# Optimization experiments

Hardware: AMD Instinct MI355X
Metric: run time of the kernel (lower is better)

Reference implementation:

```python
import jax, jax.numpy as jnp
import numpy as np

N_NODES = 100000
N_EDGES = 1600000
F_IN = 256
DIM = 128
N_CLASSES = 16


def gcn_conv(x, W, b, src, dst, num_nodes):
    # PyG GCNConv: add self-loops, symmetric normalization D^-1/2 (A+I) D^-1/2,
    # linear transform then scatter-add aggregation at destination nodes.
    loops = jnp.arange(num_nodes)
    s = jnp.concatenate([src, loops])
    d = jnp.concatenate([dst, loops])
    deg = jax.ops.segment_sum(jnp.ones(d.shape[0], dtype=x.dtype), d, num_segments=num_nodes)
    dinv = jnp.where(deg > 0, jax.lax.rsqrt(deg), jnp.zeros_like(deg))
    norm = dinv[s] * dinv[d]                       # [E+N]
    h = x @ W                                      # [N, out] transform-then-propagate
    msg = h[s] * norm[:, None]                     # gather + scale
    out = jax.ops.segment_sum(msg, d, num_segments=num_nodes)  # scatter-add
    return out + b


def setup_inputs() -> dict:
    key = jax.random.key(0)
    k1, k2, k3, k4 = jax.random.split(key, 4)
    x = jax.random.normal(k1, (N_NODES, F_IN), dtype=jnp.float32)
    edge_index = jax.random.randint(k2, (2, N_EDGES), 0, N_NODES, dtype=jnp.int64)
    W1 = jax.random.normal(k3, (F_IN, DIM), dtype=jnp.float32) * 0.05
    b1 = jnp.zeros((DIM,), dtype=jnp.float32)
    W2 = jax.random.normal(k4, (DIM, N_CLASSES), dtype=jnp.float32) * 0.05
    b2 = jnp.zeros((N_CLASSES,), dtype=jnp.float32)
    return {"x": x, "edge_index": edge_index, "W1": W1, "b1": b1, "W2": W2, "b2": b2}


def reference(x, edge_index, W1, b1, W2, b2):
    # Gcn.forward with num_layers=2 (gcs empty), eval-mode dropout (identity)
    src, dst = edge_index[0], edge_index[1]
    n = x.shape[0]
    h = jax.nn.relu(gcn_conv(x, W1, b1, src, dst, n))
    logits = gcn_conv(h, W2, b2, src, dst, n)
    return jax.nn.log_softmax(logits, axis=-1)
```

## Files before the change

kernel.cpp:

```cpp
#include <hip/hip_runtime.h>
#include <hip/hip_bf16.h>

#define F_IN   256
#define DIM    128
#define NCLS   16
#define BSH    9
#define NBMAX  256
#define CAP    10240
#define PCAP   18432

typedef short bf16x8 __attribute__((ext_vector_type(8)));
typedef float f32x4  __attribute__((ext_vector_type(4)));
typedef float f32x2  __attribute__((ext_vector_type(2)));

__device__ __forceinline__ unsigned short f2bf(float f) {
    union { float f; unsigned u; } v; v.f = f;
    unsigned r = v.u + 0x7fffu + ((v.u >> 16) & 1u);
    return (unsigned short)(r >> 16);
}
__device__ __forceinline__ float bflo(unsigned v) { return __uint_as_float(v << 16); }
__device__ __forceinline__ float bfhi(unsigned v) { return __uint_as_float(v & 0xffff0000u); }

__global__ void init_kernel(const float* __restrict__ W1, unsigned short* __restrict__ W1f,
                            int* __restrict__ bucketCur,
                            unsigned* __restrict__ h1dummy, unsigned* __restrict__ h2dummy,
                            float* __restrict__ dinv, int N) {
    int t = blockIdx.x * blockDim.x + threadIdx.x;
    if (blockIdx.x == 0) {
        bucketCur[threadIdx.x] = threadIdx.x * CAP;
        if (threadIdx.x < 32) h1dummy[threadIdx.x] = 0;
        else if (threadIdx.x < 40) h2dummy[threadIdx.x - 32] = 0;
        else if (threadIdx.x == 40) dinv[N] = 0.f;
    }
    if (t >= 8 * 32 * 16 * 8) return;
    int j = t & 7, c = (t >> 3) & 15, g = (t >> 7) & 31, f = t >> 12;
    W1f[t] = f2bf(W1[(g * 8 + j) * DIM + f * 16 + c]);
}

__global__ __launch_bounds__(1024) void part_kernel(const int* __restrict__ src,
                                                    const int* __restrict__ dst,
                                                    int* __restrict__ bucketCur,
                                                    int2* __restrict__ pairs, int E) {
    __shared__ int hist[NBMAX];
    __shared__ int pos[NBMAX];
    int t = threadIdx.x;
    int base = blockIdx.x * 8192;
    int s[8], d[8];
#pragma unroll
    for (int k = 0; k < 8; k++) {
        int i = base + k * 1024 + t;
        bool v = (i < E);
        s[k] = v ? src[i] : 0;
        d[k] = v ? dst[i] : -1;
    }
    if (t < NBMAX) hist[t] = 0;
    __syncthreads();
#pragma unroll
    for (int k = 0; k < 8; k++)
        if (d[k] >= 0) atomicAdd(&hist[d[k] >> BSH], 1);
    __syncthreads();
    if (t < NBMAX && hist[t]) pos[t] = atomicAdd(&bucketCur[t], hist[t]);
    __syncthreads();
#pragma unroll
    for (int k = 0; k < 8; k++)
        if (d[k] >= 0) {
            int p = atomicAdd(&pos[d[k] >> BSH], 1);
            pairs[p] = make_int2(s[k], d[k]);
        }
}

__global__ __launch_bounds__(512) void csr_gemm_kernel(
        const int2* __restrict__ pairs, const int* __restrict__ bucketCur,
        int* __restrict__ rowInfo, float* __restrict__ dinv, int* __restrict__ col,
        const float* __restrict__ X, const unsigned short* __restrict__ W1f,
        unsigned char* __restrict__ H1, int N, int nbCsr) {
    __shared__ int sh[16384];
    int t = threadIdx.x;

    if (blockIdx.x < nbCsr) {
        int* cnt  = sh;
        int* part = sh + 512;
        int b = blockIdx.x;
        int n0 = b << BSH;
        int nn = N - n0; if (nn > 512) nn = 512;
        int in0 = b * CAP;
        int inEnd = bucketCur[b];
        int out0 = b * PCAP;

        cnt[t] = 0;
        __syncthreads();
        for (int p = in0 + t; p < inEnd; p += 512)
            atomicAdd(&cnt[pairs[p].y - n0], 1);
        __syncthreads();

        int c0 = cnt[t];
        int p0 = (c0 + 15) & ~15;
        part[t] = p0;
        __syncthreads();
        for (int off = 1; off < 512; off <<= 1) {
            int u = (t >= off) ? part[t - off] : 0;
            __syncthreads();
            part[t] += u;
            __syncthreads();
        }
        int e0 = out0 + part[t] - p0;
        __syncthreads();
        if (t < nn) {
            rowInfo[n0 + t] = ((e0 >> 4) << 12) | (p0 >> 4);
            dinv[n0 + t] = rsqrtf((float)(c0 + 1));
        }
        cnt[t] = e0;
        __syncthreads();

        for (int p = in0 + t; p < inEnd; p += 512) {
            int2 e = pairs[p];
            int q = atomicAdd(&cnt[e.y - n0], 1);
            col[q] = e.x;
        }
        __syncthreads();
        if (t < nn) for (int q = c0; q < p0; q++) col[e0 + q] = N;
    } else {
        int gb = blockIdx.x - nbCsr;
        int wm = t >> 6, l = t & 63;
        int lr = l & 15, lg = l >> 4;
        int bm = gb * 128 + wm * 16;

        int r = bm + lr;
        r = (r < N) ? r : (N - 1);
        const float* xp = X + (size_t)r * F_IN + lg * 8;

        float4 u[16];
#pragma unroll
        for (int s = 0; s < 8; s++) {
            u[2 * s + 0] = *(const float4*)(xp + s * 32);
            u[2 * s + 1] = *(const float4*)(xp + s * 32 + 4);
        }

        uint4* wv = (uint4*)sh;
        const uint4* wg = (const uint4*)W1f;
#pragma unroll
        for (int i = 0; i < 8; i++) wv[t + i * 512] = wg[t + i * 512];
        __syncthreads();
        const unsigned short* w1s = (const unsigned short*)sh;

        f32x4 acc[8];
#pragma unroll
        for (int f = 0; f < 8; f++) acc[f] = (f32x4){0.f, 0.f, 0.f, 0.f};

#pragma unroll
        for (int s = 0; s < 8; s++) {
            float4 u0 = u[2 * s + 0];
            float4 u1 = u[2 * s + 1];
            bf16x8 a;
            a[0] = (short)f2bf(u0.x); a[1] = (short)f2bf(u0.y);
            a[2] = (short)f2bf(u0.z); a[3] = (short)f2bf(u0.w);
            a[4] = (short)f2bf(u1.x); a[5] = (short)f2bf(u1.y);
            a[6] = (short)f2bf(u1.z); a[7] = (short)f2bf(u1.w);
#pragma unroll
            for (int f = 0; f < 8; f++) {
                bf16x8 b = *(const bf16x8*)(w1s + ((((f * 32 + s * 4 + lg) * 16) + lr) << 3));
                acc[f] = __builtin_amdgcn_mfma_f32_16x16x32_bf16(a, b, acc[f], 0, 0, 0);
            }
        }
#pragma unroll
        for (int rr = 0; rr < 4; rr++) {
            int row = bm + lg * 4 + rr;
            if (row < N) {
                int w0 = __builtin_amdgcn_cvt_pk_fp8_f32(acc[0][rr], acc[1][rr], 0, false);
                w0 = __builtin_amdgcn_cvt_pk_fp8_f32(acc[2][rr], acc[3][rr], w0, true);
                int w1 = __builtin_amdgcn_cvt_pk_fp8_f32(acc[4][rr], acc[5][rr], 0, false);
                w1 = __builtin_amdgcn_cvt_pk_fp8_f32(acc[6][rr], acc[7][rr], w1, true);
                uint2 pk; pk.x = (unsigned)w0; pk.y = (unsigned)w1;
                *(uint2*)(H1 + ((size_t)row << 7) + lr * 8) = pk;
            }
        }
    }
}

__global__ __launch_bounds__(256, 8) void agg1_kernel(const unsigned char* __restrict__ H1,
                                                      const int* __restrict__ rowInfo,
                                                      const int* __restrict__ col,
                                                      const float* __restrict__ dinv,
                                                      const float* __restrict__ b1,
                                                      const float* __restrict__ W2,
                                                      unsigned short* __restrict__ H2, int N) {
    __shared__ f32x4 a_lds4[4][32];
    int tid = threadIdx.x;
    int wave = tid >> 6, lane = tid & 63;
    int d = blockIdx.x * 4 + wave;
    int half = lane >> 5;
    int li = lane & 31;
    unsigned kb4 = (unsigned)li * 4;

    float di = 0.f;
    if (d < N) {
        di = dinv[d];
        unsigned sg = *(const unsigned*)(H1 + (((unsigned)d << 7) | kb4));
        if (half) sg = 0u;
        f32x2 dsp = {di, di};
        f32x2 acc01 = __builtin_amdgcn_cvt_pk_f32_fp8((int)sg, false) * dsp;
        f32x2 acc23 = __builtin_amdgcn_cvt_pk_f32_fp8((int)sg, true) * dsp;

        int info = rowInfo[d];
        int jb = (info >> 12) << 4;
        int jend = jb + ((info & 0xFFF) << 4);
        for (int j0 = jb; j0 < jend; j0 += 64) {
            int cnt = jend - j0; if (cnt > 64) cnt = 64;
            int eidx = col[j0 + lane];
            if ((unsigned)eidx > (unsigned)N) eidx = N;
            float dv = dinv[eidx];
            for (int kk = 0; kk < cnt; kk += 16) {
                int sA = __shfl(eidx, kk + 0 + half),  sB = __shfl(eidx, kk + 2 + half);
                int sC = __shfl(eidx, kk + 4 + half),  sD = __shfl(eidx, kk + 6 + half);
                int sE = __shfl(eidx, kk + 8 + half),  sF = __shfl(eidx, kk + 10 + half);
                int sG = __shfl(eidx, kk + 12 + half), sH = __shfl(eidx, kk + 14 + half);
                float vA = __shfl(dv, kk + 0 + half),  vB = __shfl(dv, kk + 2 + half);
                float vC = __shfl(dv, kk + 4 + half),  vD = __shfl(dv, kk + 6 + half);
                float vE = __shfl(dv, kk + 8 + half),  vF = __shfl(dv, kk + 10 + half);
                float vG = __shfl(dv, kk + 12 + half), vH = __shfl(dv, kk + 14 + half);
                unsigned gA = *(const unsigned*)(H1 + (((unsigned)sA << 7) | kb4));
                unsigned gB = *(const unsigned*)(H1 + (((unsigned)sB << 7) | kb4));
                unsigned gC = *(const unsigned*)(H1 + (((unsigned)sC << 7) | kb4));
                unsigned gD = *(const unsigned*)(H1 + (((unsigned)sD << 7) | kb4));
                unsigned gE = *(const unsigned*)(H1 + (((unsigned)sE << 7) | kb4));
                unsigned gF = *(const unsigned*)(H1 + (((unsigned)sF << 7) | kb4));
                unsigned gG = *(const unsigned*)(H1 + (((unsigned)sG << 7) | kb4));
                unsigned gH = *(const unsigned*)(H1 + (((unsigned)sH << 7) | kb4));
                f32x2 wA = {vA, vA}, wB = {vB, vB}, wC = {vC, vC}, wD = {vD, vD};
                f32x2 wE = {vE, vE}, wF = {vF, vF}, wG = {vG, vG}, wH = {vH, vH};
                acc01 += __builtin_amdgcn_cvt_pk_f32_fp8((int)gA, false) * wA;
                acc23 += __builtin_amdgcn_cvt_pk_f32_fp8((int)gA, true)  * wA;
                acc01 += __builtin_amdgcn_cvt_pk_f32_fp8((int)gB, false) * wB;
                acc23 += __builtin_amdgcn_cvt_pk_f32_fp8((int)gB, true)  * wB;
                acc01 += __builtin_amdgcn_cvt_pk_f32_fp8((int)gC, false) * wC;
                acc23 += __builtin_amdgcn_cvt_pk_f32_fp8((int)gC, true)  * wC;
                acc01 += __builtin_amdgcn_cvt_pk_f32_fp8((int)gD, false) * wD;
                acc23 += __builtin_amdgcn_cvt_pk_f32_fp8((int)gD, true)  * wD;
                acc01 += __builtin_amdgcn_cvt_pk_f32_fp8((int)gE, false) * wE;
                acc23 += __builtin_amdgcn_cvt_pk_f32_fp8((int)gE, true)  * wE;
                acc01 += __builtin_amdgcn_cvt_pk_f32_fp8((int)gF, false) * wF;
                acc23 += __builtin_amdgcn_cvt_pk_f32_fp8((int)gF, true)  * wF;
                acc01 += __builtin_amdgcn_cvt_pk_f32_fp8((int)gG, false) * wG;
                acc23 += __builtin_amdgcn_cvt_pk_f32_fp8((int)gG, true)  * wG;
                acc01 += __builtin_amdgcn_cvt_pk_f32_fp8((int)gH, false) * wH;
                acc23 += __builtin_amdgcn_cvt_pk_f32_fp8((int)gH, true)  * wH;
            }
        }
        acc01.x += __shfl_xor(acc01.x, 32);
        acc01.y += __shfl_xor(acc01.y, 32);
        acc23.x += __shfl_xor(acc23.x, 32);
        acc23.y += __shfl_xor(acc23.y, 32);
        if (half == 0) {
            int p0 = li * 4;
            int f0 = ((p0 & 7) << 4) | (p0 >> 3);
            int f1 = (((p0 + 1) & 7) << 4) | ((p0 + 1) >> 3);
            int f2 = (((p0 + 2) & 7) << 4) | ((p0 + 2) >> 3);
            int f3 = (((p0 + 3) & 7) << 4) | ((p0 + 3) >> 3);
            f32x4 a;
            a[0] = fmaxf(fmaf(acc01.x, di, b1[f0]), 0.f);
            a[1] = fmaxf(fmaf(acc01.y, di, b1[f1]), 0.f);
            a[2] = fmaxf(fmaf(acc23.x, di, b1[f2]), 0.f);
            a[3] = fmaxf(fmaf(acc23.y, di, b1[f3]), 0.f);
            a_lds4[wave][li] = a;
        }
    }
    __syncthreads();
    if (d < N) {
        int c = lane & 15, kg = lane >> 4;
        const float* a_ldsf = (const float*)a_lds4[wave];
        const float* w2b = W2 + kg * 64 + c;
        float p = 0.f;
#pragma unroll
        for (int i = 0; i < 32; i++) {
            int w2off = ((i & 7) << 8) + ((i >> 3) << 4);
            p = fmaf(a_ldsf[kg * 32 + i], w2b[w2off], p);
        }
        p += __shfl_xor(p, 16);
        p += __shfl_xor(p, 32);
        if (lane < 16) H2[(size_t)d * NCLS + c] = f2bf(p * di);
    }
}

__global__ __launch_bounds__(256, 8) void agg2_kernel(const unsigned short* __restrict__ H2,
                                                      const int* __restrict__ rowInfo,
                                                      const int* __restrict__ col,
                                                      const float* __restrict__ dinv,
                                                      const float* __restrict__ b2,
                                                      float* __restrict__ OUT, int N) {
    int tid = threadIdx.x;
    int g = tid >> 3, q = tid & 7;
    int d = blockIdx.x * 32 + g;
    if (d >= N) return;
    unsigned cb = (unsigned)q * 4;
    const char* H2b = (const char*)H2;
    float di = dinv[d];
    unsigned u = *(const unsigned*)(H2b + (((unsigned)d << 5) | cb));
    f32x2 acc; acc.x = bflo(u); acc.y = bfhi(u);
    int info = rowInfo[d];
    int jb = (info >> 12) << 4;
    int jend = jb + ((info & 0xFFF) << 4);
    for (int j = jb; j < jend; j += 8) {
        unsigned u0 = *(const unsigned*)(H2b + (((unsigned)col[j + 0] << 5) | cb));
        unsigned u1 = *(const unsigned*)(H2b + (((unsigned)col[j + 1] << 5) | cb));
        unsigned u2 = *(const unsigned*)(H2b + (((unsigned)col[j + 2] << 5) | cb));
        unsigned u3 = *(const unsigned*)(H2b + (((unsigned)col[j + 3] << 5) | cb));
        unsigned u4 = *(const unsigned*)(H2b + (((unsigned)col[j + 4] << 5) | cb));
        unsigned u5 = *(const unsigned*)(H2b + (((unsigned)col[j + 5] << 5) | cb));
        unsigned u6 = *(const unsigned*)(H2b + (((unsigned)col[j + 6] << 5) | cb));
        unsigned u7 = *(const unsigned*)(H2b + (((unsigned)col[j + 7] << 5) | cb));
        f32x2 v0; v0.x = bflo(u0); v0.y = bfhi(u0);
        f32x2 v1; v1.x = bflo(u1); v1.y = bfhi(u1);
        f32x2 v2; v2.x = bflo(u2); v2.y = bfhi(u2);
        f32x2 v3; v3.x = bflo(u3); v3.y = bfhi(u3);
        f32x2 v4; v4.x = bflo(u4); v4.y = bfhi(u4);
        f32x2 v5; v5.x = bflo(u5); v5.y = bfhi(u5);
        f32x2 v6; v6.x = bflo(u6); v6.y = bfhi(u6);
        f32x2 v7; v7.x = bflo(u7); v7.y = bfhi(u7);
        acc += ((v0 + v1) + (v2 + v3)) + ((v4 + v5) + (v6 + v7));
    }
    float l0 = fmaf(acc.x, di, b2[q * 2]);
    float l1 = fmaf(acc.y, di, b2[q * 2 + 1]);
    float m = fmaxf(l0, l1);
    m = fmaxf(m, __shfl_xor(m, 1, 8));
    m = fmaxf(m, __shfl_xor(m, 2, 8));
    m = fmaxf(m, __shfl_xor(m, 4, 8));
    float e = __expf(l0 - m) + __expf(l1 - m);
    e += __shfl_xor(e, 1, 8);
    e += __shfl_xor(e, 2, 8);
    e += __shfl_xor(e, 4, 8);
    float ls = __logf(e);
    float2 o; o.x = l0 - m - ls; o.y = l1 - m - ls;
    *(float2*)(OUT + ((size_t)d << 4) + q * 2) = o;
}

extern "C" void kernel_launch(void* const* d_in, const int* in_sizes, int n_in,
                              void* d_out, int out_size, void* d_ws, size_t ws_size,
                              hipStream_t stream) {
    const float* x  = (const float*)d_in[0];
    const int*   ei = (const int*)d_in[1];
    const float* W1 = (const float*)d_in[2];
    const float* b1 = (const float*)d_in[3];
    const float* W2 = (const float*)d_in[4];
    const float* b2 = (const float*)d_in[5];
    float* out = (float*)d_out;

    const int N = in_sizes[0] / F_IN;
    const int E = in_sizes[1] / 2;
    const int* src = ei;
    const int* dst = ei + E;
    const int nb = (N + (1 << BSH) - 1) >> BSH;

    char* ws = (char*)d_ws;
    size_t off = 0;
    auto alloc = [&](size_t bytes) {
        size_t o = off;
        off += (bytes + 255) & ~(size_t)255;
        return (void*)(ws + o);
    };
    int*            bucketCur   = (int*)alloc(NBMAX * 4);
    int*            rowInfo     = (int*)alloc((size_t)N * 4);
    float*          dinv        = (float*)alloc((size_t)(N + 1) * 4);
    int*            colw        = (int*)alloc((size_t)NBMAX * PCAP * 4);
    unsigned short* w1f         = (unsigned short*)alloc(32768 * 2);
    unsigned short* h2          = (unsigned short*)alloc((size_t)(N + 1) * NCLS * 2);
    int2*           pairs       = (int2*)alloc((size_t)NBMAX * CAP * 8);
    unsigned char*  h1          = (unsigned char*)alloc((size_t)(N + 1) * DIM);
    (void)ws_size;

    const int gridE = (E + 8191) / 8192;

    init_kernel<<<128, 256, 0, stream>>>(W1, w1f, bucketCur,
                                         (unsigned*)(h1 + (size_t)N * DIM),
                                         (unsigned*)(h2 + (size_t)N * NCLS),
                                         dinv, N);
    part_kernel<<<gridE, 1024, 0, stream>>>(src, dst, bucketCur, pairs, E);
    csr_gemm_kernel<<<nb + (N + 127) / 128, 512, 0, stream>>>(pairs, bucketCur, rowInfo, dinv, colw,
                                                              x, w1f, h1, N, nb);
    agg1_kernel<<<(N + 3) / 4, 256, 0, stream>>>(h1, rowInfo, colw, dinv, b1, W2, h2, N);
    agg2_kernel<<<(N + 31) / 32, 256, 0, stream>>>(h2, rowInfo, colw, dinv, b2, out, N);
}
```

Measured before the change: 137.7 us.

## Fuse init into partition kernel and halve GEMM shared memory via two-phase W1 load

Merges the W1 conversion/init work into the edge partition kernel as extra blocks, replacing the cursor-initialised bucket offsets with zeroed counters set by a memset plus a per-bucket base. The GEMM path now stages W1 into shared memory in two halves, reducing the shared allocation from 64KB to 32KB to allow more resident blocks. This costs an extra barrier and reload in the GEMM and keeps a memset op in the stream.

Result: slower. 141.3 us (+2.6%).

```diff
diff --git a/kernel.cpp b/kernel.cpp
--- a/kernel.cpp
+++ b/kernel.cpp
@@ -21,29 +21,29 @@
 __device__ __forceinline__ float bflo(unsigned v) { return __uint_as_float(v << 16); }
 __device__ __forceinline__ float bfhi(unsigned v) { return __uint_as_float(v & 0xffff0000u); }
 
-__global__ void init_kernel(const float* __restrict__ W1, unsigned short* __restrict__ W1f,
-                            int* __restrict__ bucketCur,
-                            unsigned* __restrict__ h1dummy, unsigned* __restrict__ h2dummy,
-                            float* __restrict__ dinv, int N) {
-    int t = blockIdx.x * blockDim.x + threadIdx.x;
-    if (blockIdx.x == 0) {
-        bucketCur[threadIdx.x] = threadIdx.x * CAP;
-        if (threadIdx.x < 32) h1dummy[threadIdx.x] = 0;
-        else if (threadIdx.x < 40) h2dummy[threadIdx.x - 32] = 0;
-        else if (threadIdx.x == 40) dinv[N] = 0.f;
-    }
-    if (t >= 8 * 32 * 16 * 8) return;
-    int j = t & 7, c = (t >> 3) & 15, g = (t >> 7) & 31, f = t >> 12;
-    W1f[t] = f2bf(W1[(g * 8 + j) * DIM + f * 16 + c]);
-}
-
-__global__ __launch_bounds__(1024) void part_kernel(const int* __restrict__ src,
-                                                    const int* __restrict__ dst,
-                                                    int* __restrict__ bucketCur,
-                                                    int2* __restrict__ pairs, int E) {
+__global__ __launch_bounds__(1024) void part_init_kernel(
+        const int* __restrict__ src, const int* __restrict__ dst,
+        int* __restrict__ bucketCnt, int2* __restrict__ pairs, int E,
+        const float* __restrict__ W1, unsigned short* __restrict__ W1f,
+        unsigned* __restrict__ h1dummy, unsigned* __restrict__ h2dummy,
+        float* __restrict__ dinv, int N, int nbPart) {
+    int t = threadIdx.x;
+    if (blockIdx.x >= nbPart) {
+        int gb = blockIdx.x - nbPart;
+        if (gb == 0) {
+            if (t < 32) h1dummy[t] = 0;
+            else if (t < 40) h2dummy[t - 32] = 0;
+            else if (t == 40) dinv[N] = 0.f;
+        }
+        int tg = gb * 1024 + t;
+        if (tg < 8 * 32 * 16 * 8) {
+            int j = tg & 7, c = (tg >> 3) & 15, g = (tg >> 7) & 31, f = tg >> 12;
+            W1f[tg] = f2bf(W1[(g * 8 + j) * DIM + f * 16 + c]);
+        }
+        return;
+    }
     __shared__ int hist[NBMAX];
     __shared__ int pos[NBMAX];
-    int t = threadIdx.x;
     int base = blockIdx.x * 8192;
     int s[8], d[8];
 #pragma unroll
@@ -59,7 +59,7 @@
     for (int k = 0; k < 8; k++)
         if (d[k] >= 0) atomicAdd(&hist[d[k] >> BSH], 1);
     __syncthreads();
-    if (t < NBMAX && hist[t]) pos[t] = atomicAdd(&bucketCur[t], hist[t]);
+    if (t < NBMAX && hist[t]) pos[t] = t * CAP + atomicAdd(&bucketCnt[t], hist[t]);
     __syncthreads();
 #pragma unroll
     for (int k = 0; k < 8; k++)
@@ -70,11 +70,11 @@
 }
 
 __global__ __launch_bounds__(512) void csr_gemm_kernel(
-        const int2* __restrict__ pairs, const int* __restrict__ bucketCur,
+        const int2* __restrict__ pairs, const int* __restrict__ bucketCnt,
         int* __restrict__ rowInfo, float* __restrict__ dinv, int* __restrict__ col,
         const float* __restrict__ X, const unsigned short* __restrict__ W1f,
         unsigned char* __restrict__ H1, int N, int nbCsr) {
-    __shared__ int sh[16384];
+    __shared__ int sh[8192];
     int t = threadIdx.x;
 
     if (blockIdx.x < nbCsr) {
@@ -84,7 +84,7 @@
         int n0 = b << BSH;
         int nn = N - n0; if (nn > 512) nn = 512;
         int in0 = b * CAP;
-        int inEnd = bucketCur[b];
+        int inEnd = in0 + bucketCnt[b];
         int out0 = b * PCAP;
 
         cnt[t] = 0;
@@ -136,30 +136,34 @@
             u[2 * s + 1] = *(const float4*)(xp + s * 32 + 4);
         }
 
+        f32x4 acc[8];
+#pragma unroll
+        for (int f = 0; f < 8; f++) acc[f] = (f32x4){0.f, 0.f, 0.f, 0.f};
+
         uint4* wv = (uint4*)sh;
-        const uint4* wg = (const uint4*)W1f;
-#pragma unroll
-        for (int i = 0; i < 8; i++) wv[t + i * 512] = wg[t + i * 512];
-        __syncthreads();
         const unsigned short* w1s = (const unsigned short*)sh;
 
-        f32x4 acc[8];
-#pragma unroll
-        for (int f = 0; f < 8; f++) acc[f] = (f32x4){0.f, 0.f, 0.f, 0.f};
-
-#pragma unroll
-        for (int s = 0; s < 8; s++) {
-            float4 u0 = u[2 * s + 0];
-            float4 u1 = u[2 * s + 1];
-            bf16x8 a;
-            a[0] = (short)f2bf(u0.x); a[1] = (short)f2bf(u0.y);
-            a[2] = (short)f2bf(u0.z); a[3] = (short)f2bf(u0.w);
-            a[4] = (short)f2bf(u1.x); a[5] = (short)f2bf(u1.y);
-            a[6] = (short)f2bf(u1.z); a[7] = (short)f2bf(u1.w);
-#pragma unroll
-            for (int f = 0; f < 8; f++) {
-                bf16x8 b = *(const bf16x8*)(w1s + ((((f * 32 + s * 4 + lg) * 16) + lr) << 3));
-                acc[f] = __builtin_amdgcn_mfma_f32_16x16x32_bf16(a, b, acc[f], 0, 0, 0);
+#pragma unroll
+        for (int h = 0; h < 2; h++) {
+            if (h) __syncthreads();
+            const uint4* wg = (const uint4*)W1f + h * 2048;
+#pragma unroll
+            for (int i = 0; i < 4; i++) wv[t + i * 512] = wg[t + i * 512];
+            __syncthreads();
+#pragma unroll
+            for (int s = 0; s < 8; s++) {
+                float4 u0 = u[2 * s + 0];
+                float4 u1 = u[2 * s + 1];
+                bf16x8 a;
+                a[0] = (short)f2bf(u0.x); a[1] = (short)f2bf(u0.y);
+                a[2] = (short)f2bf(u0.z); a[3] = (short)f2bf(u0.w);
+                a[4] = (short)f2bf(u1.x); a[5] = (short)f2bf(u1.y);
+                a[6] = (short)f2bf(u1.z); a[7] = (short)f2bf(u1.w);
+#pragma unroll
+                for (int f = 0; f < 4; f++) {
+                    bf16x8 b = *(const bf16x8*)(w1s + ((((f * 32 + s * 4 + lg) * 16) + lr) << 3));
+                    acc[h * 4 + f] = __builtin_amdgcn_mfma_f32_16x16x32_bf16(a, b, acc[h * 4 + f], 0, 0, 0);
+                }
             }
         }
 #pragma unroll
@@ -357,7 +361,7 @@
         off += (bytes + 255) & ~(size_t)255;
         return (void*)(ws + o);
     };
-    int*            bucketCur   = (int*)alloc(NBMAX * 4);
+    int*            bucketCnt   = (int*)alloc(NBMAX * 4);
     int*            rowInfo     = (int*)alloc((size_t)N * 4);
     float*          dinv        = (float*)alloc((size_t)(N + 1) * 4);
     int*            colw        = (int*)alloc((size_t)NBMAX * PCAP * 4);
@@ -368,13 +372,15 @@
     (void)ws_size;
 
     const int gridE = (E + 8191) / 8192;
-
-    init_kernel<<<128, 256, 0, stream>>>(W1, w1f, bucketCur,
-                                         (unsigned*)(h1 + (size_t)N * DIM),
-                                         (unsigned*)(h2 + (size_t)N * NCLS),
-                                         dinv, N);
-    part_kernel<<<gridE, 1024, 0, stream>>>(src, dst, bucketCur, pairs, E);
-    csr_gemm_kernel<<<nb + (N + 127) / 128, 512, 0, stream>>>(pairs, bucketCur, rowInfo, dinv, colw,
+    const int initB = 32;
+
+    hipMemsetAsync(bucketCnt, 0, NBMAX * 4, stream);
+    part_init_kernel<<<gridE + initB, 1024, 0, stream>>>(src, dst, bucketCnt, pairs, E,
+                                                         W1, w1f,
+                                                         (unsigned*)(h1 + (size_t)N * DIM),
+                                                         (unsigned*)(h2 + (size_t)N * NCLS),
+                                                         dinv, N, gridE);
+    csr_gemm_kernel<<<nb + (N + 127) / 128, 512, 0, stream>>>(pairs, bucketCnt, rowInfo, dinv, colw,
                                                               x, w1f, h1, N, nb);
     agg1_kernel<<<(N + 3) / 4, 256, 0, stream>>>(h1, rowInfo, colw, dinv, b1, W2, h2, N);
     agg2_kernel<<<(N + 31) / 32, 256, 0, stream>>>(h2, rowInfo, colw, dinv, b2, out, N);
```
